# Kernel tuning notes

Measured on AMD Instinct MI355X. Metric: run time of the kernel, lower is better.

## Reference

```python
import jax, jax.numpy as jnp
import numpy as np

USERNUM = 8192
ITEMNUM = 8192
DIM = 256
EPS_NORM = 1e-8   # torch.cosine_similarity default eps
CLAMP_MIN = 1e-6
CLAMP_MAX = 1.0


def setup_inputs() -> dict:
    key = jax.random.key(0)
    ks = jax.random.split(key, 12)
    N = USERNUM + ITEMNUM
    s = 1.0 / np.sqrt(DIM)
    return {
        "A": jax.random.uniform(ks[0], (N, N), dtype=jnp.float32) * (2.0 / N),
        "features": jax.random.normal(ks[1], (N, DIM), dtype=jnp.float32),
        "Wg": jax.random.normal(ks[2], (DIM, DIM), dtype=jnp.float32) * s,
        "bg": jnp.zeros((DIM,), dtype=jnp.float32),
        "uW1": jax.random.normal(ks[3], (DIM, DIM), dtype=jnp.float32) * s,
        "ub1": jnp.zeros((DIM,), dtype=jnp.float32),
        "uW2": jax.random.normal(ks[4], (DIM, DIM), dtype=jnp.float32) * s,
        "ub2": jnp.zeros((DIM,), dtype=jnp.float32),
        "iW1": jax.random.normal(ks[5], (DIM, DIM), dtype=jnp.float32) * s,
        "ib1": jnp.zeros((DIM,), dtype=jnp.float32),
        "iW2": jax.random.normal(ks[6], (DIM, DIM), dtype=jnp.float32) * s,
        "ib2": jnp.zeros((DIM,), dtype=jnp.float32),
    }


def _mlp(h, W1, b1, W2, b2):
    return jax.nn.relu(h @ W1 + b1) @ W2 + b2


def reference(A, features, Wg, bg, uW1, ub1, uW2, ub2, iW1, ib1, iW2, ib2):
    # GCN layer: relu(A @ X @ W + b)  -> [N, DIM]
    x = jax.nn.relu((A @ features) @ Wg + bg)
    user = x[:USERNUM]
    item = x[USERNUM:]
    u = _mlp(user, uW1, ub1, uW2, ub2)   # [usernum, DIM]
    it = _mlp(item, iW1, ib1, iW2, ib2)  # [itemnum, DIM]
    # Fused L2-normalize + GEMM replaces the per-row cosine_similarity loop.
    un = u / jnp.maximum(jnp.linalg.norm(u, axis=1, keepdims=True), EPS_NORM)
    itn = it / jnp.maximum(jnp.linalg.norm(it, axis=1, keepdims=True), EPS_NORM)
    sim = un @ itn.T                      # [usernum, itemnum]
    return jnp.clip(sim, CLAMP_MIN, CLAMP_MAX)
```

## Files before the change

### kernel.cpp

```cpp
#include <hip/hip_runtime.h>
#include <hip/hip_bf16.h>

using f32x4 = __attribute__((ext_vector_type(4))) float;
using s16x8 = __attribute__((ext_vector_type(8))) short;
using i32x4 = __attribute__((ext_vector_type(4))) int;

#define NTOT 16384
#define NUSER 8192
#define DIM 256

__device__ __forceinline__ unsigned short f2bf(float f) {
  union { float f; unsigned u; } v; v.f = f;
  unsigned r = v.u + 0x7FFFu + ((v.u >> 16) & 1u);
  return (unsigned short)(r >> 16);
}

__device__ __forceinline__ unsigned pack2bf(float x, float y) {
  float2 t; t.x = x; t.y = y;
  __hip_bfloat162 h = __float22bfloat162_rn(t);
  union { __hip_bfloat162 h; unsigned u; } cv; cv.h = h;
  return cv.u;
}

__device__ __forceinline__ void gload_lds16(const void* g, void* l) {
  __builtin_amdgcn_global_load_lds(
      (const __attribute__((address_space(1))) unsigned int*)g,
      (__attribute__((address_space(3))) unsigned int*)l, 16, 0, 0);
}

__global__ __launch_bounds__(256) void transpose_cvt(const float* __restrict__ src,
                                                     unsigned short* __restrict__ dst,
                                                     int K, int N) {
  __shared__ float tile[64][65];
  const int k0 = blockIdx.x * 64, n0 = blockIdx.y * 64;
  const int t = threadIdx.x;
#pragma unroll
  for (int i = 0; i < 16; i++) {
    int idx = i * 256 + t, r = idx >> 6, c = idx & 63;
    tile[r][c] = src[(size_t)(k0 + r) * N + n0 + c];
  }
  __syncthreads();
#pragma unroll
  for (int i = 0; i < 16; i++) {
    int idx = i * 256 + t, r = idx >> 6, c = idx & 63;
    dst[(size_t)(n0 + r) * K + k0 + c] = f2bf(tile[c][r]);
  }
}

__global__ __launch_bounds__(256) void transpose_w5(const float* __restrict__ w0,
                                                    const float* __restrict__ w1,
                                                    const float* __restrict__ w2,
                                                    const float* __restrict__ w3,
                                                    const float* __restrict__ w4,
                                                    unsigned short* __restrict__ dstbase) {
  __shared__ float tile[64][65];
  const float* srcs[5] = {w0, w1, w2, w3, w4};
  const float* src = srcs[blockIdx.z];
  unsigned short* dst = dstbase + (size_t)blockIdx.z * 65536;
  const int k0 = blockIdx.x * 64, n0 = blockIdx.y * 64;
  const int t = threadIdx.x;
#pragma unroll
  for (int i = 0; i < 16; i++) {
    int idx = i * 256 + t, r = idx >> 6, c = idx & 63;
    tile[r][c] = src[(size_t)(k0 + r) * 256 + n0 + c];
  }
  __syncthreads();
#pragma unroll
  for (int i = 0; i < 16; i++) {
    int idx = i * 256 + t, r = idx >> 6, c = idx & 63;
    dst[(size_t)(n0 + r) * 256 + k0 + c] = f2bf(tile[c][r]);
  }
}

__global__ __launch_bounds__(512) void gemm1(const float* __restrict__ A,
                                             const unsigned short* __restrict__ Ft,
                                             float* __restrict__ F1p) {
  __shared__ char smem[80 * 1024];
  char* const Ab0 = smem;
  char* const Bb0 = smem + 8 * 1024;
  char* const Ab1 = smem + 40 * 1024;
  char* const Bb1 = smem + 48 * 1024;

  const int tid = threadIdx.x;
  const int l = tid & 63, w = tid >> 6;
  const int wm = w >> 2, wn = w & 3;
  const int lr = l & 15, lk = l >> 4;

  const int lin = blockIdx.x;
  const int xcd = lin & 7, slot = lin >> 3;
  const int ks = xcd >> 2;
  const int mblk = (xcd & 3) * 64 + slot;
  const int m0 = mblk * 64;
  const size_t ks0 = (size_t)ks * 8192;
  float* out = F1p + (size_t)ks * NTOT * DIM;

  const int ar = tid >> 3, ac = tid & 7;
  const float* asrc = A + (size_t)(m0 + ar) * NTOT + ks0 + ac * 8;
  const int aoff = ar * 128 + ((ac * 16) ^ ((ar & 7) << 4));

  const int brin = l >> 3;
  const int bldso = w * 4096;
  const char* bsrc = (const char*)Ft + (size_t)(w * 32 + brin) * (NTOT * 2) +
                     ks0 * 2 + (((l & 7) * 16) ^ (brin << 4));

  f32x4 zero = {0.f, 0.f, 0.f, 0.f};
  f32x4 acc[2][4];
#pragma unroll
  for (int i = 0; i < 2; i++)
#pragma unroll
    for (int j = 0; j < 4; j++) acc[i][j] = zero;

  f32x4 av0, av1;

  auto loadA = [&](int t) {
    av0 = *(const f32x4*)(asrc + t * 64);
    av1 = *(const f32x4*)(asrc + t * 64 + 4);
  };
  auto writeA = [&](char* Ab) {
    i32x4 p;
    p.x = (int)pack2bf(av0.x, av0.y);
    p.y = (int)pack2bf(av0.z, av0.w);
    p.z = (int)pack2bf(av1.x, av1.y);
    p.w = (int)pack2bf(av1.z, av1.w);
    *(i32x4*)(Ab + aoff) = p;
  };
  auto issueB = [&](int t, char* Bb) {
#pragma unroll
    for (int i = 0; i < 4; i++)
      gload_lds16(bsrc + (size_t)i * 8 * (NTOT * 2) + t * 128,
                  Bb + bldso + i * 1024);
  };
  auto compute = [&](const char* Ab, const char* Bb) {
#pragma unroll
    for (int kh = 0; kh < 2; kh++) {
      s16x8 af[2], bf[4];
#pragma unroll
      for (int mt = 0; mt < 2; mt++) {
        int r = wm * 32 + mt * 16 + lr;
        int off = r * 128 + ((kh * 64 + lk * 16) ^ ((r & 7) << 4));
        af[mt] = *(const s16x8*)(Ab + off);
      }
#pragma unroll
      for (int nt = 0; nt < 4; nt++) {
        int n = wn * 64 + nt * 16 + lr;
        int off = n * 128 + ((kh * 64 + lk * 16) ^ ((n & 7) << 4));
        bf[nt] = *(const s16x8*)(Bb + off);
      }
#pragma unroll
      for (int mt = 0; mt < 2; mt++)
#pragma unroll
        for (int nt = 0; nt < 4; nt++)
          acc[mt][nt] = __builtin_amdgcn_mfma_f32_16x16x32_bf16(af[mt], bf[nt],
                                                                acc[mt][nt], 0, 0, 0);
    }
  };

  loadA(0);
  issueB(0, Bb0);
  writeA(Ab0);
  __syncthreads();

  for (int t = 0; t < 128; t += 2) {
    issueB(t + 1, Bb1);
    loadA(t + 1);
    compute(Ab0, Bb0);
    writeA(Ab1);
    __syncthreads();
    if (t + 2 < 128) {
      issueB(t + 2, Bb0);
      loadA(t + 2);
    }
    compute(Ab1, Bb1);
    if (t + 2 < 128) writeA(Ab0);
    __syncthreads();
  }

#pragma unroll
  for (int mt = 0; mt < 2; mt++) {
    int rbase = m0 + wm * 32 + mt * 16 + lk * 4;
#pragma unroll
    for (int nt = 0; nt < 4; nt++) {
      int c = wn * 64 + nt * 16 + lr;
#pragma unroll
      for (int j = 0; j < 4; j++)
        out[(size_t)(rbase + j) * DIM + c] = acc[mt][nt][j];
    }
  }
}

__global__ __launch_bounds__(512) void mlp_in(const float* __restrict__ P,
                                              const unsigned short* __restrict__ WT,
                                              const float* __restrict__ bias,
                                              unsigned short* __restrict__ out) {
  __shared__ char smem[40 * 1024];
  char* Ab = smem;
  char* Bb = smem + 8 * 1024;
  const int tid = threadIdx.x, l = tid & 63, w = tid >> 6;
  const int wm = w >> 2, wn = w & 3;
  const int m0 = blockIdx.x * 64;
  const int arow = tid >> 4, ac4 = tid & 15;
  const int bn = tid >> 3, bg = tid & 7;
  const int lr = l & 15, lk = l >> 4;

  f32x4 zero = {0.f, 0.f, 0.f, 0.f};
  f32x4 acc[2][4];
#pragma unroll
  for (int i = 0; i < 2; i++)
#pragma unroll
    for (int j = 0; j < 4; j++) acc[i][j] = zero;

  for (int step = 0; step < 4; step++) {
#pragma unroll
    for (int i = 0; i < 2; i++) {
      int r = i * 32 + arow;
      size_t gi = (size_t)(m0 + r) * DIM + step * 64 + ac4 * 4;
      f32x4 v = *(const f32x4*)(P + gi);
      v += *(const f32x4*)(P + (size_t)NTOT * DIM + gi);
      unsigned lo = pack2bf(v.x, v.y);
      unsigned hi = pack2bf(v.z, v.w);
      int off = (r * 128 + ac4 * 8) ^ ((r & 7) << 4);
      *(unsigned long long*)(Ab + off) =
          (unsigned long long)lo | ((unsigned long long)hi << 32);
    }
#pragma unroll
    for (int i = 0; i < 4; i++) {
      int n = i * 64 + bn;
      i32x4 v = *(const i32x4*)(WT + (size_t)n * DIM + step * 64 + bg * 8);
      int off = (n * 128 + bg * 16) ^ ((n & 7) << 4);
      *(i32x4*)(Bb + off) = v;
    }
    __syncthreads();
#pragma unroll
    for (int kh = 0; kh < 2; kh++) {
      s16x8 af[2], bfr[4];
#pragma unroll
      for (int mt = 0; mt < 2; mt++) {
        int r = wm * 32 + mt * 16 + lr;
        int off = (r * 128 + kh * 64 + lk * 16) ^ ((r & 7) << 4);
        af[mt] = *(const s16x8*)(Ab + off);
      }
#pragma unroll
      for (int nt = 0; nt < 4; nt++) {
        int n = wn * 64 + nt * 16 + lr;
        int off = (n * 128 + kh * 64 + lk * 16) ^ ((n & 7) << 4);
        bfr[nt] = *(const s16x8*)(Bb + off);
      }
#pragma unroll
      for (int mt = 0; mt < 2; mt++)
#pragma unroll
        for (int nt = 0; nt < 4; nt++)
          acc[mt][nt] = __builtin_amdgcn_mfma_f32_16x16x32_bf16(af[mt], bfr[nt],
                                                                acc[mt][nt], 0, 0, 0);
    }
    __syncthreads();
  }
#pragma unroll
  for (int nt = 0; nt < 4; nt++) {
    int c = wn * 64 + nt * 16 + lr;
    float b = bias[c];
#pragma unroll
    for (int mt = 0; mt < 2; mt++) {
      int rbase = m0 + wm * 32 + mt * 16 + lk * 4;
#pragma unroll
      for (int j = 0; j < 4; j++) {
        float v = fmaxf(acc[mt][nt][j] + b, 0.f);
        out[(size_t)(rbase + j) * DIM + c] = f2bf(v);
      }
    }
  }
}

__global__ __launch_bounds__(512) void mlp_hidden(const unsigned short* __restrict__ X,
                                                  const unsigned short* __restrict__ WTu,
                                                  const unsigned short* __restrict__ WTi,
                                                  const float* __restrict__ bu,
                                                  const float* __restrict__ bi,
                                                  unsigned short* __restrict__ out) {
  __shared__ char smem[40 * 1024];
  char* Ab = smem;
  char* Bb = smem + 8 * 1024;
  const int tid = threadIdx.x, l = tid & 63, w = tid >> 6;
  const int wm = w >> 2, wn = w & 3;
  const int m0 = blockIdx.x * 64;
  const unsigned short* WT = (m0 < NUSER) ? WTu : WTi;
  const float* bias = (m0 < NUSER) ? bu : bi;
  const int ar = tid >> 3, ag = tid & 7;
  const int bn = tid >> 3, bg = tid & 7;
  const int lr = l & 15, lk = l >> 4;

  f32x4 zero = {0.f, 0.f, 0.f, 0.f};
  f32x4 acc[2][4];
#pragma unroll
  for (int i = 0; i < 2; i++)
#pragma unroll
    for (int j = 0; j < 4; j++) acc[i][j] = zero;

  for (int step = 0; step < 4; step++) {
    {
      i32x4 v = *(const i32x4*)(X + (size_t)(m0 + ar) * DIM + step * 64 + ag * 8);
      int off = (ar * 128 + ag * 16) ^ ((ar & 7) << 4);
      *(i32x4*)(Ab + off) = v;
    }
#pragma unroll
    for (int i = 0; i < 4; i++) {
      int n = i * 64 + bn;
      i32x4 v = *(const i32x4*)(WT + (size_t)n * DIM + step * 64 + bg * 8);
      int off = (n * 128 + bg * 16) ^ ((n & 7) << 4);
      *(i32x4*)(Bb + off) = v;
    }
    __syncthreads();
#pragma unroll
    for (int kh = 0; kh < 2; kh++) {
      s16x8 af[2], bfr[4];
#pragma unroll
      for (int mt = 0; mt < 2; mt++) {
        int r = wm * 32 + mt * 16 + lr;
        int off = (r * 128 + kh * 64 + lk * 16) ^ ((r & 7) << 4);
        af[mt] = *(const s16x8*)(Ab + off);
      }
#pragma unroll
      for (int nt = 0; nt < 4; nt++) {
        int n = wn * 64 + nt * 16 + lr;
        int off = (n * 128 + kh * 64 + lk * 16) ^ ((n & 7) << 4);
        bfr[nt] = *(const s16x8*)(Bb + off);
      }
#pragma unroll
      for (int mt = 0; mt < 2; mt++)
#pragma unroll
        for (int nt = 0; nt < 4; nt++)
          acc[mt][nt] = __builtin_amdgcn_mfma_f32_16x16x32_bf16(af[mt], bfr[nt],
                                                                acc[mt][nt], 0, 0, 0);
    }
    __syncthreads();
  }
#pragma unroll
  for (int nt = 0; nt < 4; nt++) {
    int c = wn * 64 + nt * 16 + lr;
    float b = bias[c];
#pragma unroll
    for (int mt = 0; mt < 2; mt++) {
      int rbase = m0 + wm * 32 + mt * 16 + lk * 4;
#pragma unroll
      for (int j = 0; j < 4; j++) {
        float v = fmaxf(acc[mt][nt][j] + b, 0.f);
        out[(size_t)(rbase + j) * DIM + c] = f2bf(v);
      }
    }
  }
}

__global__ __launch_bounds__(512) void mlp_out_norm(const unsigned short* __restrict__ H,
                                                    const unsigned short* __restrict__ WTu,
                                                    const unsigned short* __restrict__ WTi,
                                                    const float* __restrict__ bu,
                                                    const float* __restrict__ bi,
                                                    unsigned short* __restrict__ un) {
  __shared__ char smem[40 * 1024];
  __shared__ float rs[64][4];
  char* Ab = smem;
  char* Bb = smem + 8 * 1024;
  const int tid = threadIdx.x, l = tid & 63, w = tid >> 6;
  const int wm = w >> 2, wn = w & 3;
  const int m0 = blockIdx.x * 64;
  const unsigned short* WT = (m0 < NUSER) ? WTu : WTi;
  const float* bias = (m0 < NUSER) ? bu : bi;
  const int ar = tid >> 3, ag = tid & 7;
  const int bn = tid >> 3, bg = tid & 7;
  const int lr = l & 15, lk = l >> 4;

  f32x4 zero = {0.f, 0.f, 0.f, 0.f};
  f32x4 acc[2][4];
#pragma unroll
  for (int i = 0; i < 2; i++)
#pragma unroll
    for (int j = 0; j < 4; j++) acc[i][j] = zero;

  for (int step = 0; step < 4; step++) {
    {
      i32x4 v = *(const i32x4*)(H + (size_t)(m0 + ar) * DIM + step * 64 + ag * 8);
      int off = (ar * 128 + ag * 16) ^ ((ar & 7) << 4);
      *(i32x4*)(Ab + off) = v;
    }
#pragma unroll
    for (int i = 0; i < 4; i++) {
      int n = i * 64 + bn;
      i32x4 v = *(const i32x4*)(WT + (size_t)n * DIM + step * 64 + bg * 8);
      int off = (n * 128 + bg * 16) ^ ((n & 7) << 4);
      *(i32x4*)(Bb + off) = v;
    }
    __syncthreads();
#pragma unroll
    for (int kh = 0; kh < 2; kh++) {
      s16x8 af[2], bfr[4];
#pragma unroll
      for (int mt = 0; mt < 2; mt++) {
        int r = wm * 32 + mt * 16 + lr;
        int off = (r * 128 + kh * 64 + lk * 16) ^ ((r & 7) << 4);
        af[mt] = *(const s16x8*)(Ab + off);
      }
#pragma unroll
      for (int nt = 0; nt < 4; nt++) {
        int n = wn * 64 + nt * 16 + lr;
        int off = (n * 128 + kh * 64 + lk * 16) ^ ((n & 7) << 4);
        bfr[nt] = *(const s16x8*)(Bb + off);
      }
#pragma unroll
      for (int mt = 0; mt < 2; mt++)
#pragma unroll
        for (int nt = 0; nt < 4; nt++)
          acc[mt][nt] = __builtin_amdgcn_mfma_f32_16x16x32_bf16(af[mt], bfr[nt],
                                                                acc[mt][nt], 0, 0, 0);
    }
    __syncthreads();
  }

  float uval[2][4][4];
  float p[2][4];
#pragma unroll
  for (int mt = 0; mt < 2; mt++)
#pragma unroll
    for (int j = 0; j < 4; j++) p[mt][j] = 0.f;
#pragma unroll
  for (int nt = 0; nt < 4; nt++) {
    int c = wn * 64 + nt * 16 + lr;
    float b = bias[c];
#pragma unroll
    for (int mt = 0; mt < 2; mt++)
#pragma unroll
      for (int j = 0; j < 4; j++) {
        float v = acc[mt][nt][j] + b;
        uval[mt][nt][j] = v;
        p[mt][j] += v * v;
      }
  }
#pragma unroll
  for (int d = 1; d < 16; d <<= 1)
#pragma unroll
    for (int mt = 0; mt < 2; mt++)
#pragma unroll
      for (int j = 0; j < 4; j++) p[mt][j] += __shfl_xor(p[mt][j], d, 64);
  if (lr == 0) {
#pragma unroll
    for (int mt = 0; mt < 2; mt++)
#pragma unroll
      for (int j = 0; j < 4; j++) rs[wm * 32 + mt * 16 + lk * 4 + j][wn] = p[mt][j];
  }
  __syncthreads();
#pragma unroll
  for (int mt = 0; mt < 2; mt++) {
    int rl = wm * 32 + mt * 16 + lk * 4;
#pragma unroll
    for (int j = 0; j < 4; j++) {
      float tot = rs[rl + j][0] + rs[rl + j][1] + rs[rl + j][2] + rs[rl + j][3];
      float inv = 1.f / fmaxf(sqrtf(tot), 1e-8f);
#pragma unroll
      for (int nt = 0; nt < 4; nt++) {
        int c = wn * 64 + nt * 16 + lr;
        un[(size_t)(m0 + rl + j) * DIM + c] = f2bf(uval[mt][nt][j] * inv);
      }
    }
  }
}

__global__ __launch_bounds__(512) void simk(const unsigned short* __restrict__ UN,
                                            float* __restrict__ out) {
  __shared__ char smem[128 * 1024];
  char* Ab = smem;
  char* Bb = smem + 64 * 1024;
  const int tid = threadIdx.x, l = tid & 63, w = tid >> 6;
  const int wm = w >> 2, wn = w & 3;
  const int lin = blockIdx.x + (blockIdx.y << 6);
  const int xcd = lin & 7, slot = lin >> 3;
  const int nblk = xcd * 8 + (slot & 7);
  const int mblk = slot >> 3;
  const int m0 = mblk * 128, n0 = nblk * 128;
  const int lr = l & 15, lk = l >> 4;
  const int sr = tid >> 5, sg = tid & 31;

#pragma unroll
  for (int i = 0; i < 8; i++) {
    int r = i * 16 + sr;
    i32x4 va = *(const i32x4*)(UN + (size_t)(m0 + r) * DIM + sg * 8);
    i32x4 vb = *(const i32x4*)(UN + (size_t)(NUSER + n0 + r) * DIM + sg * 8);
    int off = (r * 512 + sg * 16) ^ ((r & 7) << 4);
    *(i32x4*)(Ab + off) = va;
    *(i32x4*)(Bb + off) = vb;
  }
  __syncthreads();

  f32x4 zero = {0.f, 0.f, 0.f, 0.f};
  f32x4 acc[4][2];
#pragma unroll
  for (int i = 0; i < 4; i++)
#pragma unroll
    for (int j = 0; j < 2; j++) acc[i][j] = zero;

#pragma unroll
  for (int ks = 0; ks < 8; ks++) {
    s16x8 af[4], bfr[2];
#pragma unroll
    for (int mt = 0; mt < 4; mt++) {
      int r = wm * 64 + mt * 16 + lr;
      int off = (r * 512 + ks * 64 + lk * 16) ^ ((r & 7) << 4);
      af[mt] = *(const s16x8*)(Ab + off);
    }
#pragma unroll
    for (int nt = 0; nt < 2; nt++) {
      int n = wn * 32 + nt * 16 + lr;
      int off = (n * 512 + ks * 64 + lk * 16) ^ ((n & 7) << 4);
      bfr[nt] = *(const s16x8*)(Bb + off);
    }
#pragma unroll
    for (int mt = 0; mt < 4; mt++)
#pragma unroll
      for (int nt = 0; nt < 2; nt++)
        acc[mt][nt] = __builtin_amdgcn_mfma_f32_16x16x32_bf16(af[mt], bfr[nt],
                                                              acc[mt][nt], 0, 0, 0);
  }

#pragma unroll
  for (int mt = 0; mt < 4; mt++) {
    int rbase = m0 + wm * 64 + mt * 16 + lk * 4;
#pragma unroll
    for (int nt = 0; nt < 2; nt++) {
      int c = n0 + wn * 32 + nt * 16 + lr;
#pragma unroll
      for (int j = 0; j < 4; j++) {
        float v = fminf(fmaxf(acc[mt][nt][j], 1e-6f), 1.0f);
        out[(size_t)(rbase + j) * 8192 + c] = v;
      }
    }
  }
}

extern "C" void kernel_launch(void* const* d_in, const int* in_sizes, int n_in,
                              void* d_out, int out_size, void* d_ws, size_t ws_size,
                              hipStream_t stream) {
  const float* A    = (const float*)d_in[0];
  const float* feat = (const float*)d_in[1];
  const float* Wg   = (const float*)d_in[2];
  const float* bg   = (const float*)d_in[3];
  const float* uW1  = (const float*)d_in[4];
  const float* ub1  = (const float*)d_in[5];
  const float* uW2  = (const float*)d_in[6];
  const float* ub2  = (const float*)d_in[7];
  const float* iW1  = (const float*)d_in[8];
  const float* ib1  = (const float*)d_in[9];
  const float* iW2  = (const float*)d_in[10];
  const float* ib2  = (const float*)d_in[11];
  float* out = (float*)d_out;
  char* ob = (char*)d_out;

  float*          F1p  = (float*)(ob + 0);
  unsigned short* Ft   = (unsigned short*)(ob + 33554432);
  unsigned short* WT5  = (unsigned short*)(ob + 41943040);
  unsigned short* WgT  = WT5;
  unsigned short* uW1T = WT5 + 1 * 65536;
  unsigned short* uW2T = WT5 + 2 * 65536;
  unsigned short* iW1T = WT5 + 3 * 65536;
  unsigned short* iW2T = WT5 + 4 * 65536;
  unsigned short* Xb   = (unsigned short*)(ob + 41943040 + 655360);
  unsigned short* Hb   = (unsigned short*)(ob + 41943040 + 655360 + 8388608);
  unsigned short* UN   = (unsigned short*)d_ws;

  transpose_cvt<<<dim3(256, 4), 256, 0, stream>>>(feat, Ft, NTOT, DIM);
  transpose_w5<<<dim3(4, 4, 5), 256, 0, stream>>>(Wg, uW1, uW2, iW1, iW2, WT5);

  gemm1<<<dim3(512), 512, 0, stream>>>(A, Ft, F1p);
  mlp_in<<<dim3(256), 512, 0, stream>>>(F1p, WgT, bg, Xb);
  mlp_hidden<<<dim3(256), 512, 0, stream>>>(Xb, uW1T, iW1T, ub1, ib1, Hb);
  mlp_out_norm<<<dim3(256), 512, 0, stream>>>(Hb, uW2T, iW2T, ub2, ib2, UN);
  simk<<<dim3(64, 64), 512, 0, stream>>>(UN, out);
}
```

Measured before the change: 400.1 us.

## Drop split-K in gemm1, add triple-buffered LDS pipeline with nontemporal loads

Removes the two-way split-K in the A@features GEMM, so each of 256 blocks walks the full K=16384 range. The partial-sum add in mlp_in and the second partial buffer go away. The main loop becomes a three-stage LDS ring (120KB) with explicit vmcnt waits and raw barriers, keeping two tiles of loads in flight. The A stream and final stores use nontemporal hints. Halving the block count to 256 may leave some CUs idle, and the larger LDS footprint limits occupancy to one block per CU.

```diff
diff --git a/kernel.cpp b/kernel.cpp
--- a/kernel.cpp
+++ b/kernel.cpp
@@ -72,36 +72,34 @@
   }
 }
 
+struct APair { f32x4 a, b; };
+
 __global__ __launch_bounds__(512) void gemm1(const float* __restrict__ A,
                                              const unsigned short* __restrict__ Ft,
-                                             float* __restrict__ F1p) {
-  __shared__ char smem[80 * 1024];
+                                             float* __restrict__ F1) {
+  __shared__ char smem[120 * 1024];
   char* const Ab0 = smem;
-  char* const Bb0 = smem + 8 * 1024;
-  char* const Ab1 = smem + 40 * 1024;
-  char* const Bb1 = smem + 48 * 1024;
+  char* const Ab1 = smem + 8 * 1024;
+  char* const Ab2 = smem + 16 * 1024;
+  char* const Bb0 = smem + 24 * 1024;
+  char* const Bb1 = smem + 56 * 1024;
+  char* const Bb2 = smem + 88 * 1024;
 
   const int tid = threadIdx.x;
   const int l = tid & 63, w = tid >> 6;
   const int wm = w >> 2, wn = w & 3;
   const int lr = l & 15, lk = l >> 4;
 
-  const int lin = blockIdx.x;
-  const int xcd = lin & 7, slot = lin >> 3;
-  const int ks = xcd >> 2;
-  const int mblk = (xcd & 3) * 64 + slot;
-  const int m0 = mblk * 64;
-  const size_t ks0 = (size_t)ks * 8192;
-  float* out = F1p + (size_t)ks * NTOT * DIM;
+  const int m0 = blockIdx.x * 64;
 
   const int ar = tid >> 3, ac = tid & 7;
-  const float* asrc = A + (size_t)(m0 + ar) * NTOT + ks0 + ac * 8;
+  const float* asrc = A + (size_t)(m0 + ar) * NTOT + ac * 8;
   const int aoff = ar * 128 + ((ac * 16) ^ ((ar & 7) << 4));
 
   const int brin = l >> 3;
   const int bldso = w * 4096;
   const char* bsrc = (const char*)Ft + (size_t)(w * 32 + brin) * (NTOT * 2) +
-                     ks0 * 2 + (((l & 7) * 16) ^ (brin << 4));
+                     (((l & 7) * 16) ^ (brin << 4));
 
   f32x4 zero = {0.f, 0.f, 0.f, 0.f};
   f32x4 acc[2][4];
@@ -110,26 +108,26 @@
 #pragma unroll
     for (int j = 0; j < 4; j++) acc[i][j] = zero;
 
-  f32x4 av0, av1;
-
-  auto loadA = [&](int t) {
-    av0 = *(const f32x4*)(asrc + t * 64);
-    av1 = *(const f32x4*)(asrc + t * 64 + 4);
-  };
-  auto writeA = [&](char* Ab) {
-    i32x4 p;
-    p.x = (int)pack2bf(av0.x, av0.y);
-    p.y = (int)pack2bf(av0.z, av0.w);
-    p.z = (int)pack2bf(av1.x, av1.y);
-    p.w = (int)pack2bf(av1.z, av1.w);
-    *(i32x4*)(Ab + aoff) = p;
-  };
+  APair av0, av1, av2;
+
   auto issueB = [&](int t, char* Bb) {
 #pragma unroll
     for (int i = 0; i < 4; i++)
       gload_lds16(bsrc + (size_t)i * 8 * (NTOT * 2) + t * 128,
                   Bb + bldso + i * 1024);
   };
+  auto loadA = [&](int t, APair& s) {
+    s.a = __builtin_nontemporal_load((const f32x4*)(asrc + t * 64));
+    s.b = __builtin_nontemporal_load((const f32x4*)(asrc + t * 64 + 4));
+  };
+  auto writeA = [&](const APair& s, char* Ab) {
+    i32x4 p;
+    p.x = (int)pack2bf(s.a.x, s.a.y);
+    p.y = (int)pack2bf(s.a.z, s.a.w);
+    p.z = (int)pack2bf(s.b.x, s.b.y);
+    p.w = (int)pack2bf(s.b.z, s.b.w);
+    *(i32x4*)(Ab + aoff) = p;
+  };
   auto compute = [&](const char* Ab, const char* Bb) {
 #pragma unroll
     for (int kh = 0; kh < 2; kh++) {
@@ -155,25 +153,50 @@
     }
   };
 
-  loadA(0);
+#define STEP_BAR(N)                                              \
+  asm volatile("s_waitcnt vmcnt(" #N ") lgkmcnt(0)" ::: "memory"); \
+  __builtin_amdgcn_s_barrier();                                  \
+  __builtin_amdgcn_sched_barrier(0);
+
   issueB(0, Bb0);
-  writeA(Ab0);
-  __syncthreads();
-
-  for (int t = 0; t < 128; t += 2) {
-    issueB(t + 1, Bb1);
-    loadA(t + 1);
+  loadA(0, av0);
+  issueB(1, Bb1);
+  loadA(1, av1);
+  writeA(av0, Ab0);
+  STEP_BAR(6)
+
+  for (int t = 0; t < 252; t += 3) {
+    issueB(t + 2, Bb2);
+    loadA(t + 2, av2);
     compute(Ab0, Bb0);
-    writeA(Ab1);
-    __syncthreads();
-    if (t + 2 < 128) {
-      issueB(t + 2, Bb0);
-      loadA(t + 2);
-    }
+    writeA(av1, Ab1);
+    STEP_BAR(6)
+    issueB(t + 3, Bb0);
+    loadA(t + 3, av0);
     compute(Ab1, Bb1);
-    if (t + 2 < 128) writeA(Ab0);
-    __syncthreads();
-  }
+    writeA(av2, Ab2);
+    STEP_BAR(6)
+    issueB(t + 4, Bb1);
+    loadA(t + 4, av1);
+    compute(Ab2, Bb2);
+    writeA(av0, Ab0);
+    STEP_BAR(6)
+  }
+  issueB(254, Bb2);
+  loadA(254, av2);
+  compute(Ab0, Bb0);
+  writeA(av1, Ab1);
+  STEP_BAR(6)
+  issueB(255, Bb0);
+  loadA(255, av0);
+  compute(Ab1, Bb1);
+  writeA(av2, Ab2);
+  STEP_BAR(6)
+  compute(Ab2, Bb2);
+  writeA(av0, Ab0);
+  STEP_BAR(0)
+  compute(Ab0, Bb0);
+#undef STEP_BAR
 
 #pragma unroll
   for (int mt = 0; mt < 2; mt++) {
@@ -183,7 +206,8 @@
       int c = wn * 64 + nt * 16 + lr;
 #pragma unroll
       for (int j = 0; j < 4; j++)
-        out[(size_t)(rbase + j) * DIM + c] = acc[mt][nt][j];
+        __builtin_nontemporal_store(acc[mt][nt][j],
+                                    F1 + (size_t)(rbase + j) * DIM + c);
     }
   }
 }
@@ -215,7 +239,6 @@
       int r = i * 32 + arow;
       size_t gi = (size_t)(m0 + r) * DIM + step * 64 + ac4 * 4;
       f32x4 v = *(const f32x4*)(P + gi);
-      v += *(const f32x4*)(P + (size_t)NTOT * DIM + gi);
       unsigned lo = pack2bf(v.x, v.y);
       unsigned hi = pack2bf(v.z, v.w);
       int off = (r * 128 + ac4 * 8) ^ ((r & 7) << 4);
@@ -527,7 +550,7 @@
 #pragma unroll
       for (int j = 0; j < 4; j++) {
         float v = fminf(fmaxf(acc[mt][nt][j], 1e-6f), 1.0f);
-        out[(size_t)(rbase + j) * 8192 + c] = v;
+        __builtin_nontemporal_store(v, out + (size_t)(rbase + j) * 8192 + c);
       }
     }
   }
@@ -551,23 +574,23 @@
   float* out = (float*)d_out;
   char* ob = (char*)d_out;
 
-  float*          F1p  = (float*)(ob + 0);
-  unsigned short* Ft   = (unsigned short*)(ob + 33554432);
-  unsigned short* WT5  = (unsigned short*)(ob + 41943040);
+  float*          F1   = (float*)(ob + 0);
+  unsigned short* Ft   = (unsigned short*)(ob + 16777216);
+  unsigned short* WT5  = (unsigned short*)(ob + 25165824);
   unsigned short* WgT  = WT5;
   unsigned short* uW1T = WT5 + 1 * 65536;
   unsigned short* uW2T = WT5 + 2 * 65536;
   unsigned short* iW1T = WT5 + 3 * 65536;
   unsigned short* iW2T = WT5 + 4 * 65536;
-  unsigned short* Xb   = (unsigned short*)(ob + 41943040 + 655360);
-  unsigned short* Hb   = (unsigned short*)(ob + 41943040 + 655360 + 8388608);
+  unsigned short* Xb   = (unsigned short*)(ob + 25165824 + 655360);
+  unsigned short* Hb   = (unsigned short*)(ob + 25165824 + 655360 + 8388608);
   unsigned short* UN   = (unsigned short*)d_ws;
 
   transpose_cvt<<<dim3(256, 4), 256, 0, stream>>>(feat, Ft, NTOT, DIM);
   transpose_w5<<<dim3(4, 4, 5), 256, 0, stream>>>(Wg, uW1, uW2, iW1, iW2, WT5);
 
-  gemm1<<<dim3(512), 512, 0, stream>>>(A, Ft, F1p);
-  mlp_in<<<dim3(256), 512, 0, stream>>>(F1p, WgT, bg, Xb);
+  gemm1<<<dim3(256), 512, 0, stream>>>(A, Ft, F1);
+  mlp_in<<<dim3(256), 512, 0, stream>>>(F1, WgT, bg, Xb);
   mlp_hidden<<<dim3(256), 512, 0, stream>>>(Xb, uW1T, iW1T, ub1, ib1, Hb);
   mlp_out_norm<<<dim3(256), 512, 0, stream>>>(Hb, uW2T, iW2T, ub2, ib2, UN);
   simk<<<dim3(64, 64), 512, 0, stream>>>(UN, out);
```

Measured after the change: 431.5 us. 1.08x slower.

## Enlarge gemm1 M-tile to 128 and triple-buffer A/B loads in LDS

Applied to the files above, without the earlier changes.

The A@features GEMM now gives each block 128 rows instead of 64, which halves the grid to 256 blocks and halves how often the feature tiles are reloaded. It also moves from double to triple buffering, with explicit vmcnt waits and raw barriers so global loads run two stages ahead of compute. A is read with nontemporal loads, and the partial-sum and similarity outputs are written with nontemporal stores. In exchange, LDS use rises to 144KB and register pressure grows, which allows only one block per CU and may leave CUs idle with a 256-block grid on a chip with more CUs.

```diff
diff --git a/kernel.cpp b/kernel.cpp
--- a/kernel.cpp
+++ b/kernel.cpp
@@ -75,11 +75,13 @@
 __global__ __launch_bounds__(512) void gemm1(const float* __restrict__ A,
                                              const unsigned short* __restrict__ Ft,
                                              float* __restrict__ F1p) {
-  __shared__ char smem[80 * 1024];
+  __shared__ char smem[144 * 1024];
   char* const Ab0 = smem;
-  char* const Bb0 = smem + 8 * 1024;
-  char* const Ab1 = smem + 40 * 1024;
-  char* const Bb1 = smem + 48 * 1024;
+  char* const Ab1 = smem + 16 * 1024;
+  char* const Ab2 = smem + 32 * 1024;
+  char* const Bb0 = smem + 48 * 1024;
+  char* const Bb1 = smem + 80 * 1024;
+  char* const Bb2 = smem + 112 * 1024;
 
   const int tid = threadIdx.x;
   const int l = tid & 63, w = tid >> 6;
@@ -89,14 +91,19 @@
   const int lin = blockIdx.x;
   const int xcd = lin & 7, slot = lin >> 3;
   const int ks = xcd >> 2;
-  const int mblk = (xcd & 3) * 64 + slot;
-  const int m0 = mblk * 64;
+  const int mblk = (xcd & 3) * 32 + slot;
+  const int m0 = mblk * 128;
   const size_t ks0 = (size_t)ks * 8192;
   float* out = F1p + (size_t)ks * NTOT * DIM;
 
-  const int ar = tid >> 3, ac = tid & 7;
-  const float* asrc = A + (size_t)(m0 + ar) * NTOT + ks0 + ac * 8;
-  const int aoff = ar * 128 + ((ac * 16) ^ ((ar & 7) << 4));
+  const int arow = tid >> 4, ac16 = tid & 15;
+  const float* asrc = A + (size_t)(m0 + arow) * NTOT + ks0 + ac16 * 4;
+  int aoff[4];
+#pragma unroll
+  for (int j = 0; j < 4; j++) {
+    int r = j * 32 + arow;
+    aoff[j] = r * 128 + ((ac16 * 8) ^ ((r & 7) << 4));
+  }
 
   const int brin = l >> 3;
   const int bldso = w * 4096;
@@ -104,39 +111,43 @@
                      ks0 * 2 + (((l & 7) * 16) ^ (brin << 4));
 
   f32x4 zero = {0.f, 0.f, 0.f, 0.f};
-  f32x4 acc[2][4];
-#pragma unroll
-  for (int i = 0; i < 2; i++)
+  f32x4 acc[4][4];
+#pragma unroll
+  for (int i = 0; i < 4; i++)
 #pragma unroll
     for (int j = 0; j < 4; j++) acc[i][j] = zero;
 
-  f32x4 av0, av1;
-
-  auto loadA = [&](int t) {
-    av0 = *(const f32x4*)(asrc + t * 64);
-    av1 = *(const f32x4*)(asrc + t * 64 + 4);
-  };
-  auto writeA = [&](char* Ab) {
-    i32x4 p;
-    p.x = (int)pack2bf(av0.x, av0.y);
-    p.y = (int)pack2bf(av0.z, av0.w);
-    p.z = (int)pack2bf(av1.x, av1.y);
-    p.w = (int)pack2bf(av1.z, av1.w);
-    *(i32x4*)(Ab + aoff) = p;
-  };
+  struct AQuad { f32x4 v[4]; };
+  AQuad av0, av1, av2;
+
   auto issueB = [&](int t, char* Bb) {
 #pragma unroll
     for (int i = 0; i < 4; i++)
       gload_lds16(bsrc + (size_t)i * 8 * (NTOT * 2) + t * 128,
                   Bb + bldso + i * 1024);
   };
+  auto loadA = [&](int t, AQuad& s) {
+#pragma unroll
+    for (int j = 0; j < 4; j++)
+      s.v[j] = __builtin_nontemporal_load(
+          (const f32x4*)(asrc + (size_t)j * 32 * NTOT + t * 64));
+  };
+  auto writeA = [&](const AQuad& s, char* Ab) {
+#pragma unroll
+    for (int j = 0; j < 4; j++) {
+      unsigned lo = pack2bf(s.v[j].x, s.v[j].y);
+      unsigned hi = pack2bf(s.v[j].z, s.v[j].w);
+      *(unsigned long long*)(Ab + aoff[j]) =
+          (unsigned long long)lo | ((unsigned long long)hi << 32);
+    }
+  };
   auto compute = [&](const char* Ab, const char* Bb) {
 #pragma unroll
     for (int kh = 0; kh < 2; kh++) {
-      s16x8 af[2], bf[4];
-#pragma unroll
-      for (int mt = 0; mt < 2; mt++) {
-        int r = wm * 32 + mt * 16 + lr;
+      s16x8 af[4], bf[4];
+#pragma unroll
+      for (int mt = 0; mt < 4; mt++) {
+        int r = wm * 64 + mt * 16 + lr;
         int off = r * 128 + ((kh * 64 + lk * 16) ^ ((r & 7) << 4));
         af[mt] = *(const s16x8*)(Ab + off);
       }
@@ -147,7 +158,7 @@
         bf[nt] = *(const s16x8*)(Bb + off);
       }
 #pragma unroll
-      for (int mt = 0; mt < 2; mt++)
+      for (int mt = 0; mt < 4; mt++)
 #pragma unroll
         for (int nt = 0; nt < 4; nt++)
           acc[mt][nt] = __builtin_amdgcn_mfma_f32_16x16x32_bf16(af[mt], bf[nt],
@@ -155,35 +166,51 @@
     }
   };
 
-  loadA(0);
+#define STEP_BAR(N)                                                \
+  asm volatile("s_waitcnt vmcnt(" #N ") lgkmcnt(0)" ::: "memory"); \
+  __builtin_amdgcn_s_barrier();                                    \
+  __builtin_amdgcn_sched_barrier(0);
+
   issueB(0, Bb0);
-  writeA(Ab0);
-  __syncthreads();
-
-  for (int t = 0; t < 128; t += 2) {
-    issueB(t + 1, Bb1);
-    loadA(t + 1);
+  loadA(0, av0);
+  issueB(1, Bb1);
+  loadA(1, av1);
+  writeA(av0, Ab0);
+  STEP_BAR(8)
+
+  for (int t = 0; t < 126; t += 3) {
+    issueB(t + 2, Bb2);
+    loadA(t + 2, av2);
     compute(Ab0, Bb0);
-    writeA(Ab1);
-    __syncthreads();
-    if (t + 2 < 128) {
-      issueB(t + 2, Bb0);
-      loadA(t + 2);
-    }
+    writeA(av1, Ab1);
+    STEP_BAR(8)
+    issueB(t + 3, Bb0);
+    loadA(t + 3, av0);
     compute(Ab1, Bb1);
-    if (t + 2 < 128) writeA(Ab0);
-    __syncthreads();
-  }
-
-#pragma unroll
-  for (int mt = 0; mt < 2; mt++) {
-    int rbase = m0 + wm * 32 + mt * 16 + lk * 4;
+    writeA(av2, Ab2);
+    STEP_BAR(8)
+    issueB(t + 4, Bb1);
+    loadA(t + 4, av1);
+    compute(Ab2, Bb2);
+    writeA(av0, Ab0);
+    STEP_BAR(8)
+  }
+  compute(Ab0, Bb0);
+  writeA(av1, Ab1);
+  STEP_BAR(0)
+  compute(Ab1, Bb1);
+#undef STEP_BAR
+
+#pragma unroll
+  for (int mt = 0; mt < 4; mt++) {
+    int rbase = m0 + wm * 64 + mt * 16 + lk * 4;
 #pragma unroll
     for (int nt = 0; nt < 4; nt++) {
       int c = wn * 64 + nt * 16 + lr;
 #pragma unroll
       for (int j = 0; j < 4; j++)
-        out[(size_t)(rbase + j) * DIM + c] = acc[mt][nt][j];
+        __builtin_nontemporal_store(acc[mt][nt][j],
+                                    out + (size_t)(rbase + j) * DIM + c);
     }
   }
 }
@@ -527,7 +554,7 @@
 #pragma unroll
       for (int j = 0; j < 4; j++) {
         float v = fminf(fmaxf(acc[mt][nt][j], 1e-6f), 1.0f);
-        out[(size_t)(rbase + j) * 8192 + c] = v;
+        __builtin_nontemporal_store(v, out + (size_t)(rbase + j) * 8192 + c);
       }
     }
   }
@@ -566,7 +593,7 @@
   transpose_cvt<<<dim3(256, 4), 256, 0, stream>>>(feat, Ft, NTOT, DIM);
   transpose_w5<<<dim3(4, 4, 5), 256, 0, stream>>>(Wg, uW1, uW2, iW1, iW2, WT5);
 
-  gemm1<<<dim3(512), 512, 0, stream>>>(A, Ft, F1p);
+  gemm1<<<dim3(256), 512, 0, stream>>>(A, Ft, F1p);
   mlp_in<<<dim3(256), 512, 0, stream>>>(F1p, WgT, bg, Xb);
   mlp_hidden<<<dim3(256), 512, 0, stream>>>(Xb, uW1T, iW1T, ub1, ib1, Hb);
   mlp_out_norm<<<dim3(256), 512, 0, stream>>>(Hb, uW2T, iW2T, ub2, ib2, UN);
```

Result: faster. 326.9 us (-18.3%).

## Deepen A-prefetch pipeline in gemm1 and stage final output through LDS

Applied to the files above, without the earlier changes.

gemm1 now keeps two register sets for A prefetch, loading two k-tiles ahead, and replaces __syncthreads with explicit vmcnt-based waits plus barriers, with a peeled tail. A loads and partial-output stores use nontemporal hints, and launch bounds request 4 waves per SIMD. The final similarity kernel writes clamped results into padded LDS, then issues coalesced 16-byte nontemporal stores per row instead of scattered scalar stores. The aim is to hide the A-stream latency of the dominant GEMM and improve write coalescing, at the cost of extra registers and LDS traffic.

```diff
diff --git a/kernel.cpp b/kernel.cpp
--- a/kernel.cpp
+++ b/kernel.cpp
@@ -72,13 +72,15 @@
   }
 }
 
-__global__ __launch_bounds__(512) void gemm1(const float* __restrict__ A,
-                                             const unsigned short* __restrict__ Ft,
-                                             float* __restrict__ F1p) {
+struct APair { f32x4 a, b; };
+
+__global__ __launch_bounds__(512, 4) void gemm1(const float* __restrict__ A,
+                                                const unsigned short* __restrict__ Ft,
+                                                float* __restrict__ F1p) {
   __shared__ char smem[80 * 1024];
   char* const Ab0 = smem;
-  char* const Bb0 = smem + 8 * 1024;
-  char* const Ab1 = smem + 40 * 1024;
+  char* const Ab1 = smem + 8 * 1024;
+  char* const Bb0 = smem + 16 * 1024;
   char* const Bb1 = smem + 48 * 1024;
 
   const int tid = threadIdx.x;
@@ -110,26 +112,26 @@
 #pragma unroll
     for (int j = 0; j < 4; j++) acc[i][j] = zero;
 
-  f32x4 av0, av1;
-
-  auto loadA = [&](int t) {
-    av0 = *(const f32x4*)(asrc + t * 64);
-    av1 = *(const f32x4*)(asrc + t * 64 + 4);
-  };
-  auto writeA = [&](char* Ab) {
-    i32x4 p;
-    p.x = (int)pack2bf(av0.x, av0.y);
-    p.y = (int)pack2bf(av0.z, av0.w);
-    p.z = (int)pack2bf(av1.x, av1.y);
-    p.w = (int)pack2bf(av1.z, av1.w);
-    *(i32x4*)(Ab + aoff) = p;
-  };
+  APair avP, avQ;
+
   auto issueB = [&](int t, char* Bb) {
 #pragma unroll
     for (int i = 0; i < 4; i++)
       gload_lds16(bsrc + (size_t)i * 8 * (NTOT * 2) + t * 128,
                   Bb + bldso + i * 1024);
   };
+  auto loadA = [&](int t, APair& s) {
+    s.a = __builtin_nontemporal_load((const f32x4*)(asrc + t * 64));
+    s.b = __builtin_nontemporal_load((const f32x4*)(asrc + t * 64 + 4));
+  };
+  auto writeA = [&](const APair& s, char* Ab) {
+    i32x4 p;
+    p.x = (int)pack2bf(s.a.x, s.a.y);
+    p.y = (int)pack2bf(s.a.z, s.a.w);
+    p.z = (int)pack2bf(s.b.x, s.b.y);
+    p.w = (int)pack2bf(s.b.z, s.b.w);
+    *(i32x4*)(Ab + aoff) = p;
+  };
   auto compute = [&](const char* Ab, const char* Bb) {
 #pragma unroll
     for (int kh = 0; kh < 2; kh++) {
@@ -155,25 +157,45 @@
     }
   };
 
-  loadA(0);
+#define BAR_V(N)                                                   \
+  asm volatile("s_waitcnt vmcnt(" #N ") lgkmcnt(0)" ::: "memory"); \
+  __builtin_amdgcn_s_barrier();                                    \
+  __builtin_amdgcn_sched_barrier(0);
+
   issueB(0, Bb0);
-  writeA(Ab0);
-  __syncthreads();
-
-  for (int t = 0; t < 128; t += 2) {
+  loadA(0, avP);
+  writeA(avP, Ab0);
+  loadA(1, avQ);
+  BAR_V(2)
+
+  for (int t = 0; t < 124; t += 2) {
     issueB(t + 1, Bb1);
-    loadA(t + 1);
+    loadA(t + 2, avP);
     compute(Ab0, Bb0);
-    writeA(Ab1);
-    __syncthreads();
-    if (t + 2 < 128) {
-      issueB(t + 2, Bb0);
-      loadA(t + 2);
-    }
+    writeA(avQ, Ab1);
+    BAR_V(2)
+    issueB(t + 2, Bb0);
+    loadA(t + 3, avQ);
     compute(Ab1, Bb1);
-    if (t + 2 < 128) writeA(Ab0);
-    __syncthreads();
-  }
+    writeA(avP, Ab0);
+    BAR_V(2)
+  }
+  issueB(125, Bb1);
+  loadA(126, avP);
+  compute(Ab0, Bb0);
+  writeA(avQ, Ab1);
+  BAR_V(2)
+  issueB(126, Bb0);
+  loadA(127, avQ);
+  compute(Ab1, Bb1);
+  writeA(avP, Ab0);
+  BAR_V(2)
+  issueB(127, Bb1);
+  compute(Ab0, Bb0);
+  writeA(avQ, Ab1);
+  BAR_V(0)
+  compute(Ab1, Bb1);
+#undef BAR_V
 
 #pragma unroll
   for (int mt = 0; mt < 2; mt++) {
@@ -183,7 +205,8 @@
       int c = wn * 64 + nt * 16 + lr;
 #pragma unroll
       for (int j = 0; j < 4; j++)
-        out[(size_t)(rbase + j) * DIM + c] = acc[mt][nt][j];
+        __builtin_nontemporal_store(acc[mt][nt][j],
+                                    out + (size_t)(rbase + j) * DIM + c);
     }
   }
 }
@@ -518,18 +541,26 @@
                                                               acc[mt][nt], 0, 0, 0);
   }
 
-#pragma unroll
-  for (int mt = 0; mt < 4; mt++) {
-    int rbase = m0 + wm * 64 + mt * 16 + lk * 4;
-#pragma unroll
-    for (int nt = 0; nt < 2; nt++) {
-      int c = n0 + wn * 32 + nt * 16 + lr;
+  __syncthreads();
+  float* T = (float*)smem;
+#pragma unroll
+  for (int mt = 0; mt < 4; mt++)
+#pragma unroll
+    for (int nt = 0; nt < 2; nt++)
 #pragma unroll
       for (int j = 0; j < 4; j++) {
-        float v = fminf(fmaxf(acc[mt][nt][j], 1e-6f), 1.0f);
-        out[(size_t)(rbase + j) * 8192 + c] = v;
-      }
-    }
+        int row = wm * 64 + mt * 16 + lk * 4 + j;
+        int col = wn * 32 + nt * 16 + lr;
+        T[row * 132 + col] = fminf(fmaxf(acc[mt][nt][j], 1e-6f), 1.0f);
+      }
+  __syncthreads();
+  const int l5 = tid & 31, pg = tid >> 5;
+#pragma unroll
+  for (int j = 0; j < 8; j++) {
+    int row = pg * 8 + j;
+    f32x4 v = *(const f32x4*)&T[row * 132 + l5 * 4];
+    __builtin_nontemporal_store(
+        v, (f32x4*)(out + (size_t)(m0 + row) * 8192 + n0 + l5 * 4));
   }
 }
 
```

Result: no change. 398.8 us (-0.3%).
